# Optimization experiments

Measured on AMD Instinct MI355X. Metric: run time of the kernel, lower is better.

Reference implementation:

```python
import jax, jax.numpy as jnp
import numpy as np

TAU = 0.8
LAMBDA_BALANCE = 0.05
EPS = 1e-8


def setup_inputs() -> dict:
    key = jax.random.key(0)
    ks = jax.random.split(key, 8)
    B, Din, Dh, Dout, E = 8192, 1024, 2048, 1024, 8
    x = jax.random.normal(ks[0], (B, Din), jnp.float32)
    # gumbel noise for F.gumbel_softmax: g = -log(-log(U)), U~Uniform(0,1)
    u = jax.random.uniform(ks[1], (B, E), jnp.float32, 1e-6, 1.0 - 1e-6)
    gumbel = -jnp.log(-jnp.log(u))
    gate_w = jax.random.normal(ks[2], (Din, E), jnp.float32) * 0.02
    gate_b = jnp.zeros((E,), jnp.float32)
    w1 = jax.random.normal(ks[3], (E, Din, Dh), jnp.float32) * (1.0 / np.sqrt(Din))
    b1 = jnp.zeros((E, Dh), jnp.float32)
    w2 = jax.random.normal(ks[4], (E, Dh, Dout), jnp.float32) * (1.0 / np.sqrt(Dh))
    b2 = jnp.zeros((E, Dout), jnp.float32)
    return dict(x=x, gumbel=gumbel, gate_w=gate_w, gate_b=gate_b,
                w1=w1, b1=b1, w2=w2, b2=b2)


def reference(x, gumbel, gate_w, gate_b, w1, b1, w2, b2):
    # gating logits [B, E]
    logits = x @ gate_w + gate_b
    # gumbel-softmax (soft), tau=0.8 -> selection probs (selection_policy='soft')
    probs = jax.nn.softmax((logits + gumbel) / TAU, axis=1)
    # load-balancing auxiliary loss
    router_probs = jax.nn.softmax(logits / TAU, axis=1)
    importance = router_probs.mean(axis=0)  # [E]
    load = probs.mean(axis=0)               # [E]
    importance_cv = jnp.std(importance, ddof=1) / (importance.mean() + EPS)
    load_cv = jnp.std(load, ddof=1) / (load.mean() + EPS)
    E = probs.shape[1]
    switch_loss = E * jnp.sum(importance * load)
    aux_loss = (switch_loss + importance_cv + load_cv) * LAMBDA_BALANCE
    # dense all-expert MLP stack: h [E,B,Dh], eo [E,B,Dout]
    h = jax.nn.relu(jnp.einsum('bd,edh->ebh', x, w1) + b1[:, None, :])
    eo = jnp.einsum('ebh,eho->ebo', h, w2) + b2[:, None, :]
    # bmm combine: expert_outputs [B, Dout, E] @ probs [B, E, 1] -> [B, Dout]
    output = jnp.einsum('ebo,be->bo', eo, probs)
    return output, aux_loss
```

## Files before the change

### kernel.cpp

```cpp
#include <hip/hip_runtime.h>

typedef __attribute__((ext_vector_type(4))) float f4;
typedef __attribute__((ext_vector_type(8))) short s8;
typedef __attribute__((ext_vector_type(4))) unsigned short us4;

__device__ inline float b2f(unsigned int u) {
    unsigned int v = u << 16;
    float f;
    __builtin_memcpy(&f, &v, 4);
    return f;
}
__device__ inline unsigned short f2b(float f) {
    unsigned int u;
    __builtin_memcpy(&u, &f, 4);
    unsigned int r = u + 0x7fffu + ((u >> 16) & 1u);
    return (unsigned short)(r >> 16);
}
__device__ inline void async16(const void* g, void* l) {
    __builtin_amdgcn_global_load_lds(
        (const __attribute__((address_space(1))) unsigned int*)g,
        (__attribute__((address_space(3))) unsigned int*)l, 16, 0, 0);
}

#define B_ROWS 8192
#define DIN 1024
#define DH 2048
#define DOUT 1024
#define NE 8
#define NCAT 16384

#define MFMA16(a, b, c) __builtin_amdgcn_mfma_f32_16x16x32_bf16(a, b, c, 0, 0, 0)

__global__ __launch_bounds__(64) void detect_dtype(const unsigned short* __restrict__ p, int* __restrict__ flag)
{
    const int lane = threadIdx.x;
    int sane = 0;
    for (int i = lane; i < 4096; i += 64) {
        const float a = fabsf(b2f(p[i]));
        if (a > 1e-30f && a < 1e3f) sane++;
    }
    for (int off = 32; off; off >>= 1) sane += __shfl_xor(sane, off, 64);
    if (lane == 0) *flag = (sane < 3600) ? 1 : 0;
}

__global__ __launch_bounds__(256) void normalize_kernel(const void* __restrict__ src,
                                                        unsigned short* __restrict__ dst,
                                                        const int* __restrict__ flag, int n)
{
    const int i = blockIdx.x * 256 + threadIdx.x;
    if (i >= n) return;
    if (*flag) dst[i] = f2b(((const float*)src)[i]);
    else       dst[i] = ((const unsigned short*)src)[i];
}

__global__ __launch_bounds__(256) void gating_kernel(
    const unsigned short* __restrict__ x, const unsigned short* __restrict__ gum,
    const unsigned short* __restrict__ gw, const unsigned short* __restrict__ gb,
    float* __restrict__ probs, float* __restrict__ partials)
{
    const int t = threadIdx.x, wave = t >> 6, lane = t & 63;
    float sp = 0.f, sr = 0.f;
    const int base = blockIdx.x * 32 + wave * 8;
    for (int rr = 0; rr < 8; rr++) {
        const int b = base + rr;
        float acc[8];
#pragma unroll
        for (int e = 0; e < 8; e++) acc[e] = 0.f;
        for (int kk = 0; kk < 16; kk++) {
            const int k = kk * 64 + lane;
            const float xv = b2f(x[(size_t)b * DIN + k]);
            const uint4 wv = *(const uint4*)(gw + (size_t)k * 8);
            acc[0] += xv * b2f(wv.x & 0xffffu); acc[1] += xv * b2f(wv.x >> 16);
            acc[2] += xv * b2f(wv.y & 0xffffu); acc[3] += xv * b2f(wv.y >> 16);
            acc[4] += xv * b2f(wv.z & 0xffffu); acc[5] += xv * b2f(wv.z >> 16);
            acc[6] += xv * b2f(wv.w & 0xffffu); acc[7] += xv * b2f(wv.w >> 16);
        }
#pragma unroll
        for (int e = 0; e < 8; e++)
            for (int off = 32; off; off >>= 1) acc[e] += __shfl_xor(acc[e], off, 64);
        float lg[8], p1[8], p2[8];
        float m1 = -1e30f, m2 = -1e30f;
#pragma unroll
        for (int e = 0; e < 8; e++) {
            lg[e] = acc[e] + b2f(gb[e]);
            p1[e] = (lg[e] + b2f(gum[(size_t)b * 8 + e])) * 1.25f;
            p2[e] = lg[e] * 1.25f;
            m1 = fmaxf(m1, p1[e]); m2 = fmaxf(m2, p2[e]);
        }
        float s1 = 0.f, s2 = 0.f;
#pragma unroll
        for (int e = 0; e < 8; e++) {
            p1[e] = expf(p1[e] - m1); s1 += p1[e];
            p2[e] = expf(p2[e] - m2); s2 += p2[e];
        }
        const float i1 = 1.f / s1, i2 = 1.f / s2;
        if (lane < 8) {
            const float pv = p1[lane] * i1;
            probs[(size_t)b * 8 + lane] = pv;
            sp += pv;
            sr += p2[lane] * i2;
        }
    }
    __shared__ float red[4][16];
    if (lane < 8) { red[wave][lane] = sp; red[wave][8 + lane] = sr; }
    __syncthreads();
    if (t < 16)
        partials[blockIdx.x * 16 + t] = red[0][t] + red[1][t] + red[2][t] + red[3][t];
}

__global__ void aux_finalize(const float* __restrict__ partials, void* __restrict__ outp,
                             const int* __restrict__ flag)
{
    __shared__ float fin[16];
    const int t = threadIdx.x;
    if (t < 16) {
        float s = 0.f;
        for (int i = 0; i < 256; i++) s += partials[i * 16 + t];
        fin[t] = s;
    }
    __syncthreads();
    if (t == 0) {
        float ld[8], im[8];
        for (int e = 0; e < 8; e++) { ld[e] = fin[e] / 8192.f; im[e] = fin[8 + e] / 8192.f; }
        float mi = 0.f, ml = 0.f;
        for (int e = 0; e < 8; e++) { mi += im[e]; ml += ld[e]; }
        mi *= 0.125f; ml *= 0.125f;
        float vi = 0.f, vl = 0.f, sw = 0.f;
        for (int e = 0; e < 8; e++) {
            vi += (im[e] - mi) * (im[e] - mi);
            vl += (ld[e] - ml) * (ld[e] - ml);
            sw += im[e] * ld[e];
        }
        const float cvi = sqrtf(vi / 7.f) / (mi + 1e-8f);
        const float cvl = sqrtf(vl / 7.f) / (ml + 1e-8f);
        const float aux = (8.f * sw + cvi + cvl) * 0.05f;
        if (*flag) ((float*)outp)[8388608] = aux;
        else       ((unsigned short*)outp)[8388608] = f2b(aux);
    }
}

__global__ __launch_bounds__(256) void transpose_cvt(
    const void* __restrict__ src, unsigned short* __restrict__ out,
    int R, int C, int ldOut, size_t outEStride, const int* __restrict__ flag)
{
    __shared__ unsigned short tile[64][65];
    const int e = blockIdx.z;
    const size_t eoff = (size_t)e * R * C;
    unsigned short* op = out + (size_t)e * outEStride;
    const int fl = *flag;
    const int tx = threadIdx.x, ty = threadIdx.y;
    const int r0 = blockIdx.y * 64, c0 = blockIdx.x * 64;
    if (fl) {
        const float* in = (const float*)src + eoff;
#pragma unroll
        for (int i = 0; i < 16; i++) {
            const int r = ty + i * 4;
            tile[r][tx] = f2b(in[(size_t)(r0 + r) * C + c0 + tx]);
        }
    } else {
        const unsigned short* in = (const unsigned short*)src + eoff;
#pragma unroll
        for (int i = 0; i < 16; i++) {
            const int r = ty + i * 4;
            tile[r][tx] = in[(size_t)(r0 + r) * C + c0 + tx];
        }
    }
    __syncthreads();
#pragma unroll
    for (int i = 0; i < 16; i++) {
        const int c = ty + i * 4;
        op[(size_t)(c0 + c) * ldOut + r0 + tx] = tile[tx][c];
    }
}


__global__ __launch_bounds__(256, 4) void gemm_h(
    const unsigned short* __restrict__ A,
    const unsigned short* __restrict__ Bt,
    const unsigned short* __restrict__ bias,
    const float* __restrict__ probs,
    unsigned short* __restrict__ outH)
{
    constexpr int K = DIN;
    __shared__ __align__(16) char smem[32768];
    __shared__ float probsS[128];

    const int t = threadIdx.x;
    int bid = blockIdx.y * gridDim.x + blockIdx.x;
    const int cpx = (gridDim.x * gridDim.y) >> 3;
    bid = (bid & 7) * cpx + (bid >> 3);
    const int bx = bid % gridDim.x, by = bid / gridDim.x;
    const int m0 = bx * 128, n0 = by * 128;

    if (t < 128) probsS[t] = probs[(size_t)(m0 + t) * 8 + (n0 >> 11)];

    const int wave = t >> 6, lane = t & 63;
    const int wm = wave >> 1, wn = wave & 1;
    const int quad = lane >> 4, l16 = lane & 15;

    f4 acc[4][4];
#pragma unroll
    for (int i = 0; i < 4; i++)
#pragma unroll
        for (int j = 0; j < 4; j++) { acc[i][j][0] = 0.f; acc[i][j][1] = 0.f; acc[i][j][2] = 0.f; acc[i][j][3] = 0.f; }

    const int rA = t >> 2;
    const int cb = (((t & 3) ^ ((t >> 3) & 3)) * 16);
    const char* pA0 = (const char*)(A + (size_t)(m0 + rA) * K) + cb;
    const char* pA1 = pA0 + (size_t)64 * K * 2;
    const char* pB0 = (const char*)(Bt + (size_t)(n0 + rA) * K) + cb;
    const char* pB1 = pB0 + (size_t)64 * K * 2;

    const int skey = ((quad ^ ((l16 >> 1) & 3)) << 4);
    int aoff[4], boff[4];
#pragma unroll
    for (int i = 0; i < 4; i++) {
        aoff[i] = (wm * 64 + i * 16 + l16) * 64 + skey;
        boff[i] = (wn * 64 + i * 16 + l16) * 64 + skey;
    }

    {
        char* s = smem;
        async16(pA0, s + t * 16);
        async16(pA1, s + 4096 + t * 16);
        async16(pB0, s + 8192 + t * 16);
        async16(pB1, s + 12288 + t * 16);
    }
    __syncthreads();

    int cur = 0;
    for (int k0 = 0; k0 < K; k0 += 32) {
        if (k0 + 32 < K) {
            char* s = smem + (cur ^ 1) * 16384;
            const size_t kb = (size_t)(k0 + 32) * 2;
            async16(pA0 + kb, s + t * 16);
            async16(pA1 + kb, s + 4096 + t * 16);
            async16(pB0 + kb, s + 8192 + t * 16);
            async16(pB1 + kb, s + 12288 + t * 16);
        }
        const char* s = smem + cur * 16384;
        s8 av[4], bv[4];
#pragma unroll
        for (int i = 0; i < 4; i++) av[i] = *(const s8*)(s + aoff[i]);
#pragma unroll
        for (int j = 0; j < 4; j++) bv[j] = *(const s8*)(s + 8192 + boff[j]);
#pragma unroll
        for (int i = 0; i < 4; i++)
#pragma unroll
            for (int j = 0; j < 4; j++)
                acc[i][j] = MFMA16(av[i], bv[j], acc[i][j]);
        __syncthreads();
        cur ^= 1;
    }

#pragma unroll
    for (int i = 0; i < 4; i++) {
        const int lmB = wm * 64 + i * 16 + quad * 4;
#pragma unroll
        for (int j = 0; j < 4; j++) {
            const int gn = n0 + wn * 64 + j * 16 + l16;
            const float bval = b2f(bias[gn]);
#pragma unroll
            for (int r = 0; r < 4; r++) {
                const int lm = lmB + r;
                float v = acc[i][j][r] + bval;
                v = fmaxf(v, 0.f) * probsS[lm];
                outH[(size_t)(m0 + lm) * NCAT + gn] = f2b(v);
            }
        }
    }
}

__global__ __launch_bounds__(512, 4) void gemm_o3(
    const unsigned short* __restrict__ A,
    const unsigned short* __restrict__ Bt,
    float* __restrict__ partial, int rows, int klen)
{
    constexpr int K = NCAT;
    __shared__ __align__(16) char smem[49152];
    const int t = threadIdx.x;
    const int w = t >> 6, l = t & 63;
    const int l15 = l & 15, q = l >> 4;
    const int wm = w >> 2, wn = w & 3;

    const int m0 = blockIdx.x * 128, n0 = blockIdx.y * 256;
    const int kstart = blockIdx.z * klen;

    const int srow = l >> 2;
    const int gr = ((l & 3) ^ ((l >> 3) & 3)) * 8;
    const unsigned short* pa  = A  + (size_t)(m0 + w * 16 + srow) * K + kstart + gr;
    const unsigned short* pb0 = Bt + (size_t)(n0 + w * 32 + srow) * K + kstart + gr;
    const unsigned short* pb1 = pb0 + (size_t)16 * K;

    const int skey = ((q ^ ((l15 >> 1) & 3)) << 4);
    int aoff[4], boff[4];
#pragma unroll
    for (int mf = 0; mf < 4; mf++) aoff[mf] = (wm * 64 + mf * 16 + l15) * 64 + skey;
#pragma unroll
    for (int nf = 0; nf < 4; nf++) boff[nf] = (wn * 64 + nf * 16 + l15) * 64 + skey;

    f4 acc[4][4];
#pragma unroll
    for (int i = 0; i < 4; i++)
#pragma unroll
        for (int j = 0; j < 4; j++) { acc[i][j][0] = 0.f; acc[i][j][1] = 0.f; acc[i][j][2] = 0.f; acc[i][j][3] = 0.f; }

    {
        char* Ab = smem; char* Bb = smem + 8192;
        async16(pa,  Ab + w * 1024 + (l & 63) * 16);
        async16(pb0, Bb + w * 2048 + (l & 63) * 16);
        async16(pb1, Bb + w * 2048 + 1024 + (l & 63) * 16);
    }
    __syncthreads();

    int cur = 0;
    for (int k0 = 0; k0 < klen; k0 += 32) {
        if (k0 + 32 < klen) {
            char* Ab = smem + (cur ^ 1) * 24576; char* Bb = Ab + 8192;
            const int kn = k0 + 32;
            async16(pa + kn,  Ab + w * 1024 + (l & 63) * 16);
            async16(pb0 + kn, Bb + w * 2048 + (l & 63) * 16);
            async16(pb1 + kn, Bb + w * 2048 + 1024 + (l & 63) * 16);
        }
        const char* Ab = smem + cur * 24576;
        const char* Bb = Ab + 8192;
        s8 Af[4], Bf[4];
#pragma unroll
        for (int mf = 0; mf < 4; mf++) Af[mf] = *(const s8*)(Ab + aoff[mf]);
#pragma unroll
        for (int nf = 0; nf < 4; nf++) Bf[nf] = *(const s8*)(Bb + boff[nf]);
#pragma unroll
        for (int mf = 0; mf < 4; mf++)
#pragma unroll
            for (int nf = 0; nf < 4; nf++)
                acc[mf][nf] = MFMA16(Af[mf], Bf[nf], acc[mf][nf]);
        __syncthreads();
        cur ^= 1;
    }

    float* pp = partial + (size_t)blockIdx.z * rows * DOUT;
#pragma unroll
    for (int mf = 0; mf < 4; mf++) {
        const int gmB = m0 + wm * 64 + mf * 16 + q * 4;
#pragma unroll
        for (int nf = 0; nf < 4; nf++) {
            const int gn = n0 + wn * 64 + nf * 16 + l15;
#pragma unroll
            for (int r = 0; r < 4; r++)
                pp[(size_t)(gmB + r) * DOUT + gn] = acc[mf][nf][r];
        }
    }
}

__global__ __launch_bounds__(256) void out_finalize(
    const float* __restrict__ partial, const unsigned short* __restrict__ b2,
    const float* __restrict__ probs, void* __restrict__ outp, size_t outOff,
    const int* __restrict__ flag, int rows, int nks)
{
    const int i4 = (blockIdx.x * 256 + threadIdx.x) * 4;
    if (i4 >= rows * DOUT) return;
    const int m = i4 >> 10, n = i4 & (DOUT - 1);
    f4 v = *(const f4*)(partial + i4);
    for (int ks = 1; ks < nks; ks++) {
        const f4 pv = *(const f4*)(partial + (size_t)ks * rows * DOUT + i4);
        v[0] += pv[0]; v[1] += pv[1]; v[2] += pv[2]; v[3] += pv[3];
    }
    const f4 p0 = *(const f4*)(probs + (size_t)m * 8);
    const f4 p1 = *(const f4*)(probs + (size_t)m * 8 + 4);
#pragma unroll
    for (int e = 0; e < 8; e++) {
        const us4 bv = *(const us4*)(b2 + e * DOUT + n);
        const float pe = (e < 4) ? p0[e] : p1[e - 4];
        v[0] += pe * b2f(bv[0]); v[1] += pe * b2f(bv[1]);
        v[2] += pe * b2f(bv[2]); v[3] += pe * b2f(bv[3]);
    }
    const size_t oi = outOff + i4;
    if (*flag) {
        *(f4*)((float*)outp + oi) = v;
    } else {
        us4 o;
        o[0] = f2b(v[0]); o[1] = f2b(v[1]); o[2] = f2b(v[2]); o[3] = f2b(v[3]);
        *(us4*)((unsigned short*)outp + oi) = o;
    }
}

extern "C" void kernel_launch(void* const* d_in, const int* in_sizes, int n_in,
                              void* d_out, int out_size, void* d_ws, size_t ws_size,
                              hipStream_t stream)
{
    const void* x   = d_in[0];
    const void* gum = d_in[1];
    const void* gw  = d_in[2];
    const void* gb  = d_in[3];
    const void* w1  = d_in[4];
    const void* b1  = d_in[5];
    const void* w2  = d_in[6];
    const void* b2  = d_in[7];

    char* ws = (char*)d_ws;
    size_t cur = 0;
    auto alloc = [&](size_t bytes) { size_t p = cur; cur = (cur + bytes + 255) & ~(size_t)255; return p; };

    int* flag              = (int*)(ws + alloc(256));
    float* probs           = (float*)(ws + alloc(8192 * 8 * 4));
    float* partials        = (float*)(ws + alloc(256 * 16 * 4));
    unsigned short* xn     = (unsigned short*)(ws + alloc((size_t)B_ROWS * DIN * 2));
    unsigned short* gumn   = (unsigned short*)(ws + alloc((size_t)B_ROWS * 8 * 2));
    unsigned short* gwn    = (unsigned short*)(ws + alloc((size_t)DIN * 8 * 2));
    unsigned short* gbn    = (unsigned short*)(ws + alloc(8 * 2));
    unsigned short* b1n    = (unsigned short*)(ws + alloc((size_t)NE * DH * 2));
    unsigned short* b2n    = (unsigned short*)(ws + alloc((size_t)NE * DOUT * 2));
    unsigned short* w1Tcat = (unsigned short*)(ws + alloc((size_t)NCAT * DIN * 2));
    unsigned short* w2Tcat = (unsigned short*)(ws + alloc((size_t)DOUT * NCAT * 2));
    const size_t fixed = cur;

    int R = B_ROWS, KS;
    for (;;) {
        KS = 16384 / R;
        const size_t need = fixed + (size_t)R * (NCAT * 2) + (size_t)KS * R * DOUT * 4;
        if (R <= 512 || need <= ws_size) break;
        R >>= 1;
    }
    const int klen = 16384 / KS;
    unsigned short* Hcat = (unsigned short*)(ws + fixed);
    float* partial = (float*)(ws + fixed + (size_t)R * (NCAT * 2));

    detect_dtype<<<1, 64, 0, stream>>>((const unsigned short*)x, flag);

    normalize_kernel<<<(B_ROWS * DIN + 255) / 256, 256, 0, stream>>>(x, xn, flag, B_ROWS * DIN);
    normalize_kernel<<<(B_ROWS * 8 + 255) / 256, 256, 0, stream>>>(gum, gumn, flag, B_ROWS * 8);
    normalize_kernel<<<(DIN * 8 + 255) / 256, 256, 0, stream>>>(gw, gwn, flag, DIN * 8);
    normalize_kernel<<<1, 256, 0, stream>>>(gb, gbn, flag, 8);
    normalize_kernel<<<(NE * DH + 255) / 256, 256, 0, stream>>>(b1, b1n, flag, NE * DH);
    normalize_kernel<<<(NE * DOUT + 255) / 256, 256, 0, stream>>>(b2, b2n, flag, NE * DOUT);

    gating_kernel<<<256, 256, 0, stream>>>(xn, gumn, gwn, gbn, probs, partials);
    aux_finalize<<<1, 64, 0, stream>>>(partials, d_out, flag);

    transpose_cvt<<<dim3(DH / 64, DIN / 64, NE), dim3(64, 4), 0, stream>>>(
        w1, w1Tcat, DIN, DH, DIN, (size_t)DH * DIN, flag);
    transpose_cvt<<<dim3(DOUT / 64, DH / 64, NE), dim3(64, 4), 0, stream>>>(
        w2, w2Tcat, DH, DOUT, NCAT, (size_t)DH, flag);

    for (int c0 = 0; c0 < B_ROWS; c0 += R) {
        gemm_h<<<dim3(R / 128, NCAT / 128), 256, 0, stream>>>(
            xn + (size_t)c0 * DIN, w1Tcat, b1n, probs + (size_t)c0 * 8, Hcat);
        gemm_o3<<<dim3(R / 128, DOUT / 256, KS), 512, 0, stream>>>(
            Hcat, w2Tcat, partial, R, klen);
        out_finalize<<<(R * DOUT / 4 + 255) / 256, 256, 0, stream>>>(
            partial, b2n, probs + (size_t)c0 * 8, d_out, (size_t)c0 * DOUT, flag, R, KS);
    }
}
```

Baseline: 971.4 us.

## Retile output GEMM to 128x128 tiles, halve split-K, vectorize normalize

The second GEMM moves from 512-thread 128x256 tiles to 256-thread 128x128 tiles with a smaller shared-memory double buffer. The split-K factor drops from 16384/R to 8192/R, so at full batch there is no split and half as much fp32 partial data is written and read back by the finalize kernel. The input normalize/convert kernel now handles 8 elements per thread with vector loads and stores instead of one scalar element. Each GEMM block now runs a longer K loop with less B-tile reuse per block, which trades some load efficiency for lower partial-sum traffic.

```diff
diff --git a/kernel.cpp b/kernel.cpp
--- a/kernel.cpp
+++ b/kernel.cpp
@@ -43,14 +43,23 @@
     if (lane == 0) *flag = (sane < 3600) ? 1 : 0;
 }
 
-__global__ __launch_bounds__(256) void normalize_kernel(const void* __restrict__ src,
-                                                        unsigned short* __restrict__ dst,
-                                                        const int* __restrict__ flag, int n)
+__global__ __launch_bounds__(256) void normalize8(const void* __restrict__ src,
+                                                  unsigned short* __restrict__ dst,
+                                                  const int* __restrict__ flag, int n8)
 {
     const int i = blockIdx.x * 256 + threadIdx.x;
-    if (i >= n) return;
-    if (*flag) dst[i] = f2b(((const float*)src)[i]);
-    else       dst[i] = ((const unsigned short*)src)[i];
+    if (i >= n8) return;
+    if (*flag) {
+        const f4 a = ((const f4*)src)[i * 2];
+        const f4 b = ((const f4*)src)[i * 2 + 1];
+        us4 o0, o1;
+        o0[0] = f2b(a[0]); o0[1] = f2b(a[1]); o0[2] = f2b(a[2]); o0[3] = f2b(a[3]);
+        o1[0] = f2b(b[0]); o1[1] = f2b(b[1]); o1[2] = f2b(b[2]); o1[3] = f2b(b[3]);
+        ((us4*)dst)[i * 2] = o0;
+        ((us4*)dst)[i * 2 + 1] = o1;
+    } else {
+        ((s8*)dst)[i] = ((const s8*)src)[i];
+    }
 }
 
 __global__ __launch_bounds__(256) void gating_kernel(
@@ -271,83 +280,86 @@
     }
 }
 
-__global__ __launch_bounds__(512, 4) void gemm_o3(
+__global__ __launch_bounds__(256, 4) void gemm_o4(
     const unsigned short* __restrict__ A,
     const unsigned short* __restrict__ Bt,
     float* __restrict__ partial, int rows, int klen)
 {
     constexpr int K = NCAT;
-    __shared__ __align__(16) char smem[49152];
+    __shared__ __align__(16) char smem[32768];
+
     const int t = threadIdx.x;
-    const int w = t >> 6, l = t & 63;
-    const int l15 = l & 15, q = l >> 4;
-    const int wm = w >> 2, wn = w & 3;
-
-    const int m0 = blockIdx.x * 128, n0 = blockIdx.y * 256;
+    const int m0 = blockIdx.x * 128, n0 = blockIdx.y * 128;
     const int kstart = blockIdx.z * klen;
-
-    const int srow = l >> 2;
-    const int gr = ((l & 3) ^ ((l >> 3) & 3)) * 8;
-    const unsigned short* pa  = A  + (size_t)(m0 + w * 16 + srow) * K + kstart + gr;
-    const unsigned short* pb0 = Bt + (size_t)(n0 + w * 32 + srow) * K + kstart + gr;
-    const unsigned short* pb1 = pb0 + (size_t)16 * K;
-
-    const int skey = ((q ^ ((l15 >> 1) & 3)) << 4);
+    const int wave = t >> 6, lane = t & 63;
+    const int wm = wave >> 1, wn = wave & 1;
+    const int quad = lane >> 4, l16 = lane & 15;
+
+    f4 acc[4][4];
+#pragma unroll
+    for (int i = 0; i < 4; i++)
+#pragma unroll
+        for (int j = 0; j < 4; j++) { acc[i][j][0] = 0.f; acc[i][j][1] = 0.f; acc[i][j][2] = 0.f; acc[i][j][3] = 0.f; }
+
+    const int rA = t >> 2;
+    const int cb = (((t & 3) ^ ((t >> 3) & 3)) * 16);
+    const char* pA0 = (const char*)(A + (size_t)(m0 + rA) * K + kstart) + cb;
+    const char* pA1 = pA0 + (size_t)64 * K * 2;
+    const char* pB0 = (const char*)(Bt + (size_t)(n0 + rA) * K + kstart) + cb;
+    const char* pB1 = pB0 + (size_t)64 * K * 2;
+
+    const int skey = ((quad ^ ((l16 >> 1) & 3)) << 4);
     int aoff[4], boff[4];
 #pragma unroll
-    for (int mf = 0; mf < 4; mf++) aoff[mf] = (wm * 64 + mf * 16 + l15) * 64 + skey;
-#pragma unroll
-    for (int nf = 0; nf < 4; nf++) boff[nf] = (wn * 64 + nf * 16 + l15) * 64 + skey;
-
-    f4 acc[4][4];
-#pragma unroll
-    for (int i = 0; i < 4; i++)
-#pragma unroll
-        for (int j = 0; j < 4; j++) { acc[i][j][0] = 0.f; acc[i][j][1] = 0.f; acc[i][j][2] = 0.f; acc[i][j][3] = 0.f; }
+    for (int i = 0; i < 4; i++) {
+        aoff[i] = (wm * 64 + i * 16 + l16) * 64 + skey;
+        boff[i] = (wn * 64 + i * 16 + l16) * 64 + skey;
+    }
 
     {
-        char* Ab = smem; char* Bb = smem + 8192;
-        async16(pa,  Ab + w * 1024 + (l & 63) * 16);
-        async16(pb0, Bb + w * 2048 + (l & 63) * 16);
-        async16(pb1, Bb + w * 2048 + 1024 + (l & 63) * 16);
+        char* s = smem;
+        async16(pA0, s + t * 16);
+        async16(pA1, s + 4096 + t * 16);
+        async16(pB0, s + 8192 + t * 16);
+        async16(pB1, s + 12288 + t * 16);
     }
     __syncthreads();
 
     int cur = 0;
     for (int k0 = 0; k0 < klen; k0 += 32) {
         if (k0 + 32 < klen) {
-            char* Ab = smem + (cur ^ 1) * 24576; char* Bb = Ab + 8192;
-            const int kn = k0 + 32;
-            async16(pa + kn,  Ab + w * 1024 + (l & 63) * 16);
-            async16(pb0 + kn, Bb + w * 2048 + (l & 63) * 16);
-            async16(pb1 + kn, Bb + w * 2048 + 1024 + (l & 63) * 16);
-        }
-        const char* Ab = smem + cur * 24576;
-        const char* Bb = Ab + 8192;
-        s8 Af[4], Bf[4];
-#pragma unroll
-        for (int mf = 0; mf < 4; mf++) Af[mf] = *(const s8*)(Ab + aoff[mf]);
-#pragma unroll
-        for (int nf = 0; nf < 4; nf++) Bf[nf] = *(const s8*)(Bb + boff[nf]);
-#pragma unroll
-        for (int mf = 0; mf < 4; mf++)
-#pragma unroll
-            for (int nf = 0; nf < 4; nf++)
-                acc[mf][nf] = MFMA16(Af[mf], Bf[nf], acc[mf][nf]);
+            char* s = smem + (cur ^ 1) * 16384;
+            const size_t kb = (size_t)(k0 + 32) * 2;
+            async16(pA0 + kb, s + t * 16);
+            async16(pA1 + kb, s + 4096 + t * 16);
+            async16(pB0 + kb, s + 8192 + t * 16);
+            async16(pB1 + kb, s + 12288 + t * 16);
+        }
+        const char* s = smem + cur * 16384;
+        s8 av[4], bv[4];
+#pragma unroll
+        for (int i = 0; i < 4; i++) av[i] = *(const s8*)(s + aoff[i]);
+#pragma unroll
+        for (int j = 0; j < 4; j++) bv[j] = *(const s8*)(s + 8192 + boff[j]);
+#pragma unroll
+        for (int i = 0; i < 4; i++)
+#pragma unroll
+            for (int j = 0; j < 4; j++)
+                acc[i][j] = MFMA16(av[i], bv[j], acc[i][j]);
         __syncthreads();
         cur ^= 1;
     }
 
     float* pp = partial + (size_t)blockIdx.z * rows * DOUT;
 #pragma unroll
-    for (int mf = 0; mf < 4; mf++) {
-        const int gmB = m0 + wm * 64 + mf * 16 + q * 4;
-#pragma unroll
-        for (int nf = 0; nf < 4; nf++) {
-            const int gn = n0 + wn * 64 + nf * 16 + l15;
+    for (int i = 0; i < 4; i++) {
+        const int gmB = m0 + wm * 64 + i * 16 + quad * 4;
+#pragma unroll
+        for (int j = 0; j < 4; j++) {
+            const int gn = n0 + wn * 64 + j * 16 + l16;
 #pragma unroll
             for (int r = 0; r < 4; r++)
-                pp[(size_t)(gmB + r) * DOUT + gn] = acc[mf][nf][r];
+                pp[(size_t)(gmB + r) * DOUT + gn] = acc[i][j][r];
         }
     }
 }
@@ -416,23 +428,23 @@
 
     int R = B_ROWS, KS;
     for (;;) {
-        KS = 16384 / R;
+        KS = 8192 / R; if (KS < 1) KS = 1;
         const size_t need = fixed + (size_t)R * (NCAT * 2) + (size_t)KS * R * DOUT * 4;
         if (R <= 512 || need <= ws_size) break;
         R >>= 1;
     }
-    const int klen = 16384 / KS;
+    const int klen = NCAT / KS;
     unsigned short* Hcat = (unsigned short*)(ws + fixed);
     float* partial = (float*)(ws + fixed + (size_t)R * (NCAT * 2));
 
     detect_dtype<<<1, 64, 0, stream>>>((const unsigned short*)x, flag);
 
-    normalize_kernel<<<(B_ROWS * DIN + 255) / 256, 256, 0, stream>>>(x, xn, flag, B_ROWS * DIN);
-    normalize_kernel<<<(B_ROWS * 8 + 255) / 256, 256, 0, stream>>>(gum, gumn, flag, B_ROWS * 8);
-    normalize_kernel<<<(DIN * 8 + 255) / 256, 256, 0, stream>>>(gw, gwn, flag, DIN * 8);
-    normalize_kernel<<<1, 256, 0, stream>>>(gb, gbn, flag, 8);
-    normalize_kernel<<<(NE * DH + 255) / 256, 256, 0, stream>>>(b1, b1n, flag, NE * DH);
-    normalize_kernel<<<(NE * DOUT + 255) / 256, 256, 0, stream>>>(b2, b2n, flag, NE * DOUT);
+    normalize8<<<(B_ROWS * DIN / 8 + 255) / 256, 256, 0, stream>>>(x, xn, flag, B_ROWS * DIN / 8);
+    normalize8<<<(B_ROWS * 8 / 8 + 255) / 256, 256, 0, stream>>>(gum, gumn, flag, B_ROWS);
+    normalize8<<<(DIN * 8 / 8 + 255) / 256, 256, 0, stream>>>(gw, gwn, flag, DIN);
+    normalize8<<<1, 256, 0, stream>>>(gb, gbn, flag, 1);
+    normalize8<<<(NE * DH / 8 + 255) / 256, 256, 0, stream>>>(b1, b1n, flag, NE * DH / 8);
+    normalize8<<<(NE * DOUT / 8 + 255) / 256, 256, 0, stream>>>(b2, b2n, flag, NE * DOUT / 8);
 
     gating_kernel<<<256, 256, 0, stream>>>(xn, gumn, gwn, gbn, probs, partials);
     aux_finalize<<<1, 64, 0, stream>>>(partials, d_out, flag);
@@ -445,7 +457,7 @@
     for (int c0 = 0; c0 < B_ROWS; c0 += R) {
         gemm_h<<<dim3(R / 128, NCAT / 128), 256, 0, stream>>>(
             xn + (size_t)c0 * DIN, w1Tcat, b1n, probs + (size_t)c0 * 8, Hcat);
-        gemm_o3<<<dim3(R / 128, DOUT / 256, KS), 512, 0, stream>>>(
+        gemm_o4<<<dim3(R / 128, DOUT / 128, KS), 256, 0, stream>>>(
             Hcat, w2Tcat, partial, R, klen);
         out_finalize<<<(R * DOUT / 4 + 255) / 256, 256, 0, stream>>>(
             partial, b2n, probs + (size_t)c0 * 8, d_out, (size_t)c0 * DOUT, flag, R, KS);
```

Measured after the change: 1.041 ms. 7.2% more time.
